# Performance work log

Hardware: AMD Instinct MI355X
Metric: run time of the kernel (lower is better)

Reference implementation:

```python
import jax, jax.numpy as jnp
import numpy as np

N_EMBD = 1024
N_HEAD = 16
HEAD_SIZE = 64


def setup_inputs() -> dict:
    key = jax.random.key(0)
    ks = jax.random.split(key, 6)
    B, T, C, H, D = 2, 2048, N_EMBD, N_HEAD, HEAD_SIZE
    s = 1.0 / np.sqrt(C)
    x = jax.random.normal(ks[0], (B, T, C), dtype=jnp.float32)
    Wq = jax.random.normal(ks[1], (H, C, D), dtype=jnp.float32) * s
    Wk = jax.random.normal(ks[2], (H, C, D), dtype=jnp.float32) * s
    Wv = jax.random.normal(ks[3], (H, C, D), dtype=jnp.float32) * s
    Wo = jax.random.normal(ks[4], (H * D, C), dtype=jnp.float32) * (1.0 / np.sqrt(H * D))
    bo = jax.random.normal(ks[5], (C,), dtype=jnp.float32) * 0.01
    return {"x": x, "Wq": Wq, "Wk": Wk, "Wv": Wv, "Wo": Wo, "bo": bo}


def reference(x, Wq, Wk, Wv, Wo, bo):
    B, T, C = x.shape
    H, _, D = Wq.shape
    # Per-head projections, batched across heads: [B,H,T,D]
    q = jnp.einsum('btc,hcd->bhtd', x, Wq)
    k = jnp.einsum('btc,hcd->bhtd', x, Wk)
    v = jnp.einsum('btc,hcd->bhtd', x, Wv)
    # NOTE: original scales by sqrt(C) = sqrt(n_embd), not sqrt(head_size)
    scale = 1.0 / jnp.sqrt(jnp.float32(C))
    att = jnp.einsum('bhtd,bhsd->bhts', q, k) * scale  # [B,H,T,T]
    causal = jnp.tril(jnp.ones((T, T), dtype=bool))
    att = jnp.where(causal, att, -jnp.inf)
    att = jax.nn.softmax(att, axis=-1)
    # dropout omitted (eval mode / deterministic reference)
    out = jnp.einsum('bhts,bhsd->bhtd', att, v)  # [B,H,T,D]
    out = out.transpose(0, 2, 1, 3).reshape(B, T, H * D)
    return out @ Wo + bo
```

## Files before the change

### kernel.cpp

```cpp
#include <hip/hip_runtime.h>
#include <hip/hip_bf16.h>


typedef __hip_bfloat16 bf16;
typedef __bf16 v8bf __attribute__((ext_vector_type(8)));
typedef float  v4f  __attribute__((ext_vector_type(4)));
typedef unsigned long long u64;
typedef unsigned int u32;

#define MFMA16(a, b, c) __builtin_amdgcn_mfma_f32_16x16x32_bf16((a), (b), (c), 0, 0, 0)

__device__ __forceinline__ bf16 f2b(float x) { return __float2bfloat16(x); }
__device__ __forceinline__ __bf16 f2braw(float x) {
  bf16 t = __float2bfloat16(x);
  return *reinterpret_cast<__bf16*>(&t);
}
__device__ __forceinline__ unsigned short f2bu(float x) {
  bf16 t = __float2bfloat16(x);
  return *reinterpret_cast<unsigned short*>(&t);
}

__device__ __forceinline__ void load16_lds(const bf16* gptr, const bf16* lptr) {
  __builtin_amdgcn_global_load_lds(
      (const __attribute__((address_space(1))) u32*)gptr,
      (__attribute__((address_space(3))) u32*)lptr, 16, 0, 0);
}

__global__ __launch_bounds__(256) void cvt_x_kernel(
    const float* __restrict__ x, bf16* __restrict__ xb)
{
  size_t i = ((size_t)blockIdx.x * 256 + threadIdx.x) * 8;
  float4 f0 = *(const float4*)(x + i);
  float4 f1 = *(const float4*)(x + i + 4);
  v8bf v;
  v[0] = f2braw(f0.x); v[1] = f2braw(f0.y); v[2] = f2braw(f0.z); v[3] = f2braw(f0.w);
  v[4] = f2braw(f1.x); v[5] = f2braw(f1.y); v[6] = f2braw(f1.z); v[7] = f2braw(f1.w);
  *(v8bf*)(xb + i) = v;
}

__global__ __launch_bounds__(256) void transpose_qkv_kernel(
    const float* __restrict__ Wq, const float* __restrict__ Wk,
    const float* __restrict__ Wv, bf16* __restrict__ wt)
{
  __shared__ float Lt[32][33];
  const int z = blockIdx.z, p = z >> 4, h = z & 15;
  const float* ib = ((p == 0) ? Wq : (p == 1) ? Wk : Wv) + (size_t)h * 65536;
  bf16* ob = wt + (size_t)z * 65536;
  const int j0 = blockIdx.x * 32;
  const int i0 = blockIdx.y * 32;
  const int tx = threadIdx.x & 31, ty = threadIdx.x >> 5;
  #pragma unroll
  for (int r = 0; r < 4; ++r)
    Lt[ty + 8 * r][tx] = ib[(size_t)(i0 + ty + 8 * r) * 64 + j0 + tx];
  __syncthreads();
  #pragma unroll
  for (int r = 0; r < 4; ++r)
    ob[(size_t)(j0 + ty + 8 * r) * 1024 + i0 + tx] = f2b(Lt[tx][ty + 8 * r]);
}

__global__ __launch_bounds__(256) void transpose_wo_kernel(
    const float* __restrict__ in, bf16* __restrict__ outp)
{
  __shared__ float Lt[32][33];
  const int j0 = blockIdx.x * 32;
  const int i0 = blockIdx.y * 32;
  const int tx = threadIdx.x & 31, ty = threadIdx.x >> 5;
  #pragma unroll
  for (int r = 0; r < 4; ++r)
    Lt[ty + 8 * r][tx] = in[(size_t)(i0 + ty + 8 * r) * 1024 + j0 + tx];
  __syncthreads();
  #pragma unroll
  for (int r = 0; r < 4; ++r)
    outp[(size_t)(j0 + ty + 8 * r) * 1024 + i0 + tx] = f2b(Lt[tx][ty + 8 * r]);
}

__global__ __launch_bounds__(256) void qkv_gemm_kernel(
    const bf16* __restrict__ xb, const bf16* __restrict__ wt,
    bf16* __restrict__ qkv)
{
  __shared__ __align__(16) bf16 Ash[128][32];
  __shared__ __align__(16) bf16 Bsh[128][32];

  const int mt = blockIdx.x, nt = blockIdx.y;
  const int tid = threadIdx.x, w = tid >> 6, lane = tid & 63;
  const int ln = lane & 15, quad = lane >> 4;
  const int wm = w >> 1, wn = w & 1;
  const int m0 = mt * 128, n0 = nt * 128;

  const v4f vzero = {0.f, 0.f, 0.f, 0.f};
  v4f acc[4][4];
  #pragma unroll
  for (int mf = 0; mf < 4; ++mf)
    #pragma unroll
    for (int nf = 0; nf < 4; ++nf) acc[mf][nf] = vzero;

  const int srow = lane >> 2, sseg = (lane & 3) * 8;
  const bf16* ga = xb + (size_t)(m0 + 32 * w + srow) * 1024 + sseg;
  const bf16* gb = wt + (size_t)(n0 + 32 * w + srow) * 1024 + sseg;

  for (int k0 = 0; k0 < 1024; k0 += 32) {
    __syncthreads();
    load16_lds(ga + k0,             &Ash[32 * w][0]);
    load16_lds(ga + 16 * 1024 + k0, &Ash[32 * w + 16][0]);
    load16_lds(gb + k0,             &Bsh[32 * w][0]);
    load16_lds(gb + 16 * 1024 + k0, &Bsh[32 * w + 16][0]);
    __syncthreads();

    v8bf af[4], bfv[4];
    #pragma unroll
    for (int mf = 0; mf < 4; ++mf)
      af[mf] = *(const v8bf*)&Ash[wm * 64 + mf * 16 + ln][quad * 8];
    #pragma unroll
    for (int nf = 0; nf < 4; ++nf)
      bfv[nf] = *(const v8bf*)&Bsh[wn * 64 + nf * 16 + ln][quad * 8];
    #pragma unroll
    for (int mf = 0; mf < 4; ++mf)
      #pragma unroll
      for (int nf = 0; nf < 4; ++nf)
        acc[mf][nf] = MFMA16(af[mf], bfv[nf], acc[mf][nf]);
  }

  const int jcol0 = n0 + wn * 64;
  const int p = jcol0 >> 10;
  const int h = (jcol0 >> 6) & 15;
  const float scale = (p == 0) ? 0.03125f : 1.0f;

  if (p < 2) {
    bf16* base = qkv + (size_t)p * 4194304 + (size_t)h * 262144;
    #pragma unroll
    for (int mf = 0; mf < 4; ++mf)
      #pragma unroll
      for (int nf = 0; nf < 4; ++nf) {
        int d = nf * 16 + ln;
        #pragma unroll
        for (int r = 0; r < 4; ++r) {
          int m = m0 + wm * 64 + mf * 16 + quad * 4 + r;
          base[(size_t)m * 64 + d] = f2b(acc[mf][nf][r] * scale);
        }
      }
  } else {
    bf16* vb = qkv + (size_t)2 * 4194304 + (size_t)h * 262144;
    #pragma unroll
    for (int mf = 0; mf < 4; ++mf) {
      int mrow = m0 + wm * 64 + mf * 16 + quad * 4;
      int bi = mrow >> 11, t0 = mrow & 2047;
      #pragma unroll
      for (int nf = 0; nf < 4; ++nf) {
        int d = nf * 16 + ln;
        u64 pk = (u64)f2bu(acc[mf][nf][0]) |
                 ((u64)f2bu(acc[mf][nf][1]) << 16) |
                 ((u64)f2bu(acc[mf][nf][2]) << 32) |
                 ((u64)f2bu(acc[mf][nf][3]) << 48);
        *(u64*)(vb + (size_t)bi * 131072 + (size_t)d * 2048 + t0) = pk;
      }
    }
  }
}

__global__ __launch_bounds__(256) void attn_kernel(
    const bf16* __restrict__ qkv, bf16* __restrict__ att)
{
  __shared__ __align__(16) bf16 Ksh0[64][32], Ksh1[64][32];
  __shared__ __align__(16) bf16 Vsh0[64][32], Vsh1[64][32];
  __shared__ __align__(16) __bf16 Psh[4][16][72];

  const int fid = blockIdx.x;
  const int lo = fid & 255, hi = fid >> 8;
  const int mt = hi ? (15 - (lo & 15)) : (lo & 15);
  const int b = hi, h = (lo >> 4) & 15;
  const int row0 = mt * 128;

  const int tid = threadIdx.x, w = tid >> 6, lane = tid & 63;
  const int ln = lane & 15, quad = lane >> 4;

  const bf16* qbase  = qkv + (size_t)h * 262144 + (size_t)b * 131072;
  const bf16* kbase  = qbase + 4194304;
  const bf16* vtbase = qbase + 8388608;

  v8bf aq[2][2];
  #pragma unroll
  for (int mc = 0; mc < 2; ++mc)
    #pragma unroll
    for (int ks = 0; ks < 2; ++ks)
      aq[mc][ks] = *(const v8bf*)(qbase +
          (size_t)(row0 + w * 32 + mc * 16 + ln) * 64 + ks * 32 + quad * 8);

  v8bf vone;
  {
    unsigned short u = 0x3F80;
    __bf16 one_e = *reinterpret_cast<__bf16*>(&u);
    #pragma unroll
    for (int j = 0; j < 8; ++j) vone[j] = one_e;
  }

  const v4f vzero = {0.f, 0.f, 0.f, 0.f};
  v4f o[2][4], lacc[2];
  #pragma unroll
  for (int mc = 0; mc < 2; ++mc) {
    lacc[mc] = vzero;
    #pragma unroll
    for (int n = 0; n < 4; ++n) o[mc][n] = vzero;
  }

  const float NEG = -30000.0f;
  const int wrow = row0 + w * 32;
  const int wk_last = (wrow + 31) >> 6;
  const int kb_end = (row0 + 127) >> 6;

  const int srow = lane >> 2, sseg = (lane & 3) * 8;

  for (int kb = 0; kb <= kb_end; ++kb) {
    __syncthreads();
    {
      const bf16* gk = kbase + (size_t)(kb * 64 + w * 16 + srow) * 64 + sseg;
      load16_lds(gk,      &Ksh0[w * 16][0]);
      load16_lds(gk + 32, &Ksh1[w * 16][0]);
      const bf16* gv = vtbase + (size_t)(w * 16 + srow) * 2048 + kb * 64 + sseg;
      load16_lds(gv,      &Vsh0[w * 16][0]);
      load16_lds(gv + 32, &Vsh1[w * 16][0]);
    }
    __syncthreads();

    if (kb <= wk_last) {
      v8bf kf[2][4], vf[2][4];
      #pragma unroll
      for (int nf = 0; nf < 4; ++nf) {
        kf[0][nf] = *(const v8bf*)&Ksh0[nf * 16 + ln][quad * 8];
        kf[1][nf] = *(const v8bf*)&Ksh1[nf * 16 + ln][quad * 8];
        vf[0][nf] = *(const v8bf*)&Vsh0[nf * 16 + ln][quad * 8];
        vf[1][nf] = *(const v8bf*)&Vsh1[nf * 16 + ln][quad * 8];
      }

      #pragma unroll
      for (int mc = 0; mc < 2; ++mc) {
        v4f s[4];
        #pragma unroll
        for (int nf = 0; nf < 4; ++nf) s[nf] = vzero;
        #pragma unroll
        for (int ks = 0; ks < 2; ++ks)
          #pragma unroll
          for (int nf = 0; nf < 4; ++nf)
            s[nf] = MFMA16(aq[mc][ks], kf[ks][nf], s[nf]);

        if (kb == wk_last) {
          int row = wrow + mc * 16 + quad * 4;
          #pragma unroll
          for (int nf = 0; nf < 4; ++nf) {
            int col = kb * 64 + nf * 16 + ln;
            #pragma unroll
            for (int r = 0; r < 4; ++r)
              if (col > row + r) s[nf][r] = NEG;
          }
        }

        #pragma unroll
        for (int nf = 0; nf < 4; ++nf)
          #pragma unroll
          for (int r = 0; r < 4; ++r)
            Psh[w][quad * 4 + r][nf * 16 + ln] = f2braw(__expf(s[nf][r]));
        __asm__ volatile("s_waitcnt lgkmcnt(0)" ::: "memory");

        #pragma unroll
        for (int ks = 0; ks < 2; ++ks) {
          v8bf pf = *(const v8bf*)&Psh[w][ln][ks * 32 + quad * 8];
          lacc[mc] = MFMA16(pf, vone, lacc[mc]);
          #pragma unroll
          for (int nf = 0; nf < 4; ++nf)
            o[mc][nf] = MFMA16(pf, vf[ks][nf], o[mc][nf]);
        }
      }
    }
  }

  #pragma unroll
  for (int mc = 0; mc < 2; ++mc) {
    v4f inv;
    #pragma unroll
    for (int r = 0; r < 4; ++r) inv[r] = 1.0f / lacc[mc][r];
    #pragma unroll
    for (int nf = 0; nf < 4; ++nf)
      #pragma unroll
      for (int r = 0; r < 4; ++r) {
        int m = b * 2048 + wrow + mc * 16 + quad * 4 + r;
        att[(size_t)m * 1024 + h * 64 + nf * 16 + ln] = f2b(o[mc][nf][r] * inv[r]);
      }
  }
}

__global__ __launch_bounds__(256) void out_gemm_kernel(
    const bf16* __restrict__ att, const bf16* __restrict__ wot,
    const float* __restrict__ bo, float* __restrict__ out)
{
  __shared__ __align__(16) bf16 Ash[128][32];
  __shared__ __align__(16) bf16 Bsh[64][32];

  const int mt = blockIdx.x, nt = blockIdx.y;
  const int tid = threadIdx.x, w = tid >> 6, lane = tid & 63;
  const int ln = lane & 15, quad = lane >> 4;
  const int wm = w >> 1, wn = w & 1;
  const int m0 = mt * 128, n0 = nt * 64;

  const v4f vzero = {0.f, 0.f, 0.f, 0.f};
  v4f acc[4][2];
  #pragma unroll
  for (int mf = 0; mf < 4; ++mf)
    #pragma unroll
    for (int nf = 0; nf < 2; ++nf) acc[mf][nf] = vzero;

  const int srow = lane >> 2, sseg = (lane & 3) * 8;
  const bf16* ga = att + (size_t)(m0 + 32 * w + srow) * 1024 + sseg;
  const bf16* gb = wot + (size_t)(n0 + 16 * w + srow) * 1024 + sseg;

  for (int k0 = 0; k0 < 1024; k0 += 32) {
    __syncthreads();
    load16_lds(ga + k0,             &Ash[32 * w][0]);
    load16_lds(ga + 16 * 1024 + k0, &Ash[32 * w + 16][0]);
    load16_lds(gb + k0,             &Bsh[16 * w][0]);
    __syncthreads();

    v8bf af[4], bfv[2];
    #pragma unroll
    for (int mf = 0; mf < 4; ++mf)
      af[mf] = *(const v8bf*)&Ash[wm * 64 + mf * 16 + ln][quad * 8];
    #pragma unroll
    for (int nf = 0; nf < 2; ++nf)
      bfv[nf] = *(const v8bf*)&Bsh[wn * 32 + nf * 16 + ln][quad * 8];
    #pragma unroll
    for (int mf = 0; mf < 4; ++mf)
      #pragma unroll
      for (int nf = 0; nf < 2; ++nf)
        acc[mf][nf] = MFMA16(af[mf], bfv[nf], acc[mf][nf]);
  }

  #pragma unroll
  for (int nf = 0; nf < 2; ++nf) {
    int j = n0 + wn * 32 + nf * 16 + ln;
    float bias = bo[j];
    #pragma unroll
    for (int mf = 0; mf < 4; ++mf)
      #pragma unroll
      for (int r = 0; r < 4; ++r) {
        int m = m0 + wm * 64 + mf * 16 + quad * 4 + r;
        out[(size_t)m * 1024 + j] = acc[mf][nf][r] + bias;
      }
  }
}

extern "C" void kernel_launch(void* const* d_in, const int* in_sizes, int n_in,
                              void* d_out, int out_size, void* d_ws, size_t ws_size,
                              hipStream_t stream) {
  const float* x  = (const float*)d_in[0];
  const float* Wq = (const float*)d_in[1];
  const float* Wk = (const float*)d_in[2];
  const float* Wv = (const float*)d_in[3];
  const float* Wo = (const float*)d_in[4];
  const float* bo = (const float*)d_in[5];
  float* out = (float*)d_out;

  bf16* xb  = (bf16*)d_ws;
  bf16* wt  = xb + 4194304;
  bf16* wot = xb + 7340032;
  bf16* qkv = xb + 8388608;
  bf16* att = xb + 20971520;

  cvt_x_kernel<<<2048, 256, 0, stream>>>(x, xb);
  transpose_qkv_kernel<<<dim3(2, 32, 48), 256, 0, stream>>>(Wq, Wk, Wv, wt);
  transpose_wo_kernel<<<dim3(32, 32), 256, 0, stream>>>(Wo, wot);

  qkv_gemm_kernel<<<dim3(32, 24), 256, 0, stream>>>(xb, wt, qkv);
  attn_kernel<<<512, 256, 0, stream>>>(qkv, att);
  out_gemm_kernel<<<dim3(32, 16), 256, 0, stream>>>(att, wot, bo, out);
}
```

Before: 192.2 us.

## Merge prep kernels, double-buffer GEMM and attention LDS, shrink attention blocks

Combines the three preprocessing kernels (x cast, QKV weight transpose, Wo transpose) into one launch. Adds double-buffered LDS staging with prefetch of the next K tile in both GEMMs and in the attention kernel, which removes one barrier per iteration. Attention now uses 128-thread blocks over 64-row query tiles with twice as many blocks, which should improve causal load balance and occupancy. LDS use per block roughly doubles, and correctness relies on the global_load_lds writes having landed by the next barrier.

```diff
diff --git a/kernel.cpp b/kernel.cpp
--- a/kernel.cpp
+++ b/kernel.cpp
@@ -26,60 +26,59 @@
       (__attribute__((address_space(3))) u32*)lptr, 16, 0, 0);
 }
 
-__global__ __launch_bounds__(256) void cvt_x_kernel(
-    const float* __restrict__ x, bf16* __restrict__ xb)
-{
-  size_t i = ((size_t)blockIdx.x * 256 + threadIdx.x) * 8;
-  float4 f0 = *(const float4*)(x + i);
-  float4 f1 = *(const float4*)(x + i + 4);
-  v8bf v;
-  v[0] = f2braw(f0.x); v[1] = f2braw(f0.y); v[2] = f2braw(f0.z); v[3] = f2braw(f0.w);
-  v[4] = f2braw(f1.x); v[5] = f2braw(f1.y); v[6] = f2braw(f1.z); v[7] = f2braw(f1.w);
-  *(v8bf*)(xb + i) = v;
-}
-
-__global__ __launch_bounds__(256) void transpose_qkv_kernel(
+__global__ __launch_bounds__(256) void prep_kernel(
+    const float* __restrict__ x,
     const float* __restrict__ Wq, const float* __restrict__ Wk,
-    const float* __restrict__ Wv, bf16* __restrict__ wt)
+    const float* __restrict__ Wv, const float* __restrict__ Wo,
+    bf16* __restrict__ xb, bf16* __restrict__ wt, bf16* __restrict__ wot)
 {
   __shared__ float Lt[32][33];
-  const int z = blockIdx.z, p = z >> 4, h = z & 15;
-  const float* ib = ((p == 0) ? Wq : (p == 1) ? Wk : Wv) + (size_t)h * 65536;
-  bf16* ob = wt + (size_t)z * 65536;
-  const int j0 = blockIdx.x * 32;
-  const int i0 = blockIdx.y * 32;
-  const int tx = threadIdx.x & 31, ty = threadIdx.x >> 5;
-  #pragma unroll
-  for (int r = 0; r < 4; ++r)
-    Lt[ty + 8 * r][tx] = ib[(size_t)(i0 + ty + 8 * r) * 64 + j0 + tx];
-  __syncthreads();
-  #pragma unroll
-  for (int r = 0; r < 4; ++r)
-    ob[(size_t)(j0 + ty + 8 * r) * 1024 + i0 + tx] = f2b(Lt[tx][ty + 8 * r]);
-}
-
-__global__ __launch_bounds__(256) void transpose_wo_kernel(
-    const float* __restrict__ in, bf16* __restrict__ outp)
-{
-  __shared__ float Lt[32][33];
-  const int j0 = blockIdx.x * 32;
-  const int i0 = blockIdx.y * 32;
-  const int tx = threadIdx.x & 31, ty = threadIdx.x >> 5;
-  #pragma unroll
-  for (int r = 0; r < 4; ++r)
-    Lt[ty + 8 * r][tx] = in[(size_t)(i0 + ty + 8 * r) * 1024 + j0 + tx];
-  __syncthreads();
-  #pragma unroll
-  for (int r = 0; r < 4; ++r)
-    outp[(size_t)(j0 + ty + 8 * r) * 1024 + i0 + tx] = f2b(Lt[tx][ty + 8 * r]);
+  const int bid = blockIdx.x, tid = threadIdx.x;
+
+  if (bid < 2048) {
+    size_t i = ((size_t)bid * 256 + tid) * 8;
+    float4 f0 = *(const float4*)(x + i);
+    float4 f1 = *(const float4*)(x + i + 4);
+    v8bf v;
+    v[0] = f2braw(f0.x); v[1] = f2braw(f0.y); v[2] = f2braw(f0.z); v[3] = f2braw(f0.w);
+    v[4] = f2braw(f1.x); v[5] = f2braw(f1.y); v[6] = f2braw(f1.z); v[7] = f2braw(f1.w);
+    *(v8bf*)(xb + i) = v;
+    return;
+  }
+  const int tx = tid & 31, ty = tid >> 5;
+  if (bid < 5120) {
+    const int idx = bid - 2048;
+    const int z = idx >> 6, rem = idx & 63;
+    const int p = z >> 4, h = z & 15;
+    const float* ib = ((p == 0) ? Wq : (p == 1) ? Wk : Wv) + (size_t)h * 65536;
+    bf16* ob = wt + (size_t)z * 65536;
+    const int j0 = (rem & 1) * 32, i0 = (rem >> 1) * 32;
+    #pragma unroll
+    for (int r = 0; r < 4; ++r)
+      Lt[ty + 8 * r][tx] = ib[(size_t)(i0 + ty + 8 * r) * 64 + j0 + tx];
+    __syncthreads();
+    #pragma unroll
+    for (int r = 0; r < 4; ++r)
+      ob[(size_t)(j0 + ty + 8 * r) * 1024 + i0 + tx] = f2b(Lt[tx][ty + 8 * r]);
+  } else {
+    const int idx = bid - 5120;
+    const int j0 = (idx & 31) * 32, i0 = (idx >> 5) * 32;
+    #pragma unroll
+    for (int r = 0; r < 4; ++r)
+      Lt[ty + 8 * r][tx] = Wo[(size_t)(i0 + ty + 8 * r) * 1024 + j0 + tx];
+    __syncthreads();
+    #pragma unroll
+    for (int r = 0; r < 4; ++r)
+      wot[(size_t)(j0 + ty + 8 * r) * 1024 + i0 + tx] = f2b(Lt[tx][ty + 8 * r]);
+  }
 }
 
 __global__ __launch_bounds__(256) void qkv_gemm_kernel(
     const bf16* __restrict__ xb, const bf16* __restrict__ wt,
     bf16* __restrict__ qkv)
 {
-  __shared__ __align__(16) bf16 Ash[128][32];
-  __shared__ __align__(16) bf16 Bsh[128][32];
+  __shared__ __align__(16) bf16 Ash[2][128][32];
+  __shared__ __align__(16) bf16 Bsh[2][128][32];
 
   const int mt = blockIdx.x, nt = blockIdx.y;
   const int tid = threadIdx.x, w = tid >> 6, lane = tid & 63;
@@ -98,21 +97,33 @@
   const bf16* ga = xb + (size_t)(m0 + 32 * w + srow) * 1024 + sseg;
   const bf16* gb = wt + (size_t)(n0 + 32 * w + srow) * 1024 + sseg;
 
-  for (int k0 = 0; k0 < 1024; k0 += 32) {
+  {
+    load16_lds(ga,             &Ash[0][32 * w][0]);
+    load16_lds(ga + 16 * 1024, &Ash[0][32 * w + 16][0]);
+    load16_lds(gb,             &Bsh[0][32 * w][0]);
+    load16_lds(gb + 16 * 1024, &Bsh[0][32 * w + 16][0]);
+  }
+
+  for (int kt = 0; kt < 32; ++kt) {
+    const int buf = kt & 1;
     __syncthreads();
-    load16_lds(ga + k0,             &Ash[32 * w][0]);
-    load16_lds(ga + 16 * 1024 + k0, &Ash[32 * w + 16][0]);
-    load16_lds(gb + k0,             &Bsh[32 * w][0]);
-    load16_lds(gb + 16 * 1024 + k0, &Bsh[32 * w + 16][0]);
-    __syncthreads();
 
     v8bf af[4], bfv[4];
     #pragma unroll
     for (int mf = 0; mf < 4; ++mf)
-      af[mf] = *(const v8bf*)&Ash[wm * 64 + mf * 16 + ln][quad * 8];
+      af[mf] = *(const v8bf*)&Ash[buf][wm * 64 + mf * 16 + ln][quad * 8];
     #pragma unroll
     for (int nf = 0; nf < 4; ++nf)
-      bfv[nf] = *(const v8bf*)&Bsh[wn * 64 + nf * 16 + ln][quad * 8];
+      bfv[nf] = *(const v8bf*)&Bsh[buf][wn * 64 + nf * 16 + ln][quad * 8];
+
+    if (kt < 31) {
+      const int k0 = (kt + 1) * 32, nb = buf ^ 1;
+      load16_lds(ga + k0,             &Ash[nb][32 * w][0]);
+      load16_lds(ga + 16 * 1024 + k0, &Ash[nb][32 * w + 16][0]);
+      load16_lds(gb + k0,             &Bsh[nb][32 * w][0]);
+      load16_lds(gb + 16 * 1024 + k0, &Bsh[nb][32 * w + 16][0]);
+    }
+
     #pragma unroll
     for (int mf = 0; mf < 4; ++mf)
       #pragma unroll
@@ -157,18 +168,19 @@
   }
 }
 
-__global__ __launch_bounds__(256) void attn_kernel(
+__global__ __launch_bounds__(128) void attn_kernel(
     const bf16* __restrict__ qkv, bf16* __restrict__ att)
 {
-  __shared__ __align__(16) bf16 Ksh0[64][32], Ksh1[64][32];
-  __shared__ __align__(16) bf16 Vsh0[64][32], Vsh1[64][32];
-  __shared__ __align__(16) __bf16 Psh[4][16][72];
+  __shared__ __align__(16) bf16 Ksh[2][2][64][32];
+  __shared__ __align__(16) bf16 Vsh[2][2][64][32];
+  __shared__ __align__(16) __bf16 Psh[2][16][72];
 
   const int fid = blockIdx.x;
-  const int lo = fid & 255, hi = fid >> 8;
-  const int mt = hi ? (15 - (lo & 15)) : (lo & 15);
-  const int b = hi, h = (lo >> 4) & 15;
-  const int row0 = mt * 128;
+  const int mtraw = fid & 31;
+  const int mt = ((fid >> 8) & 1) ? (31 - mtraw) : mtraw;
+  const int grp = (fid >> 5) & 31;
+  const int b = grp >> 4, h = grp & 15;
+  const int row0 = mt * 64;
 
   const int tid = threadIdx.x, w = tid >> 6, lane = tid & 63;
   const int ln = lane & 15, quad = lane >> 4;
@@ -177,13 +189,14 @@
   const bf16* kbase  = qbase + 4194304;
   const bf16* vtbase = qbase + 8388608;
 
+  const int wrow = row0 + w * 32;
   v8bf aq[2][2];
   #pragma unroll
   for (int mc = 0; mc < 2; ++mc)
     #pragma unroll
     for (int ks = 0; ks < 2; ++ks)
       aq[mc][ks] = *(const v8bf*)(qbase +
-          (size_t)(row0 + w * 32 + mc * 16 + ln) * 64 + ks * 32 + quad * 8);
+          (size_t)(wrow + mc * 16 + ln) * 64 + ks * 32 + quad * 8);
 
   v8bf vone;
   {
@@ -203,74 +216,83 @@
   }
 
   const float NEG = -30000.0f;
-  const int wrow = row0 + w * 32;
-  const int wk_last = (wrow + 31) >> 6;
-  const int kb_end = (row0 + 127) >> 6;
-
+  const int kb_end = mt;
   const int srow = lane >> 2, sseg = (lane & 3) * 8;
 
+  const bf16* gk0 = kbase + (size_t)(w * 32 + srow) * 64 + sseg;
+  const bf16* gv0 = vtbase + (size_t)(w * 32 + srow) * 2048 + sseg;
+
+  #define STAGE(KB, BUF)                                                     \
+    {                                                                        \
+      const bf16* gk = gk0 + (size_t)(KB) * 64 * 64;                         \
+      load16_lds(gk,            &Ksh[BUF][0][w * 32][0]);                    \
+      load16_lds(gk + 32,       &Ksh[BUF][1][w * 32][0]);                    \
+      load16_lds(gk + 1024,     &Ksh[BUF][0][w * 32 + 16][0]);               \
+      load16_lds(gk + 1056,     &Ksh[BUF][1][w * 32 + 16][0]);               \
+      const bf16* gv = gv0 + (KB) * 64;                                      \
+      load16_lds(gv,            &Vsh[BUF][0][w * 32][0]);                    \
+      load16_lds(gv + 32,       &Vsh[BUF][1][w * 32][0]);                    \
+      load16_lds(gv + 32768,    &Vsh[BUF][0][w * 32 + 16][0]);               \
+      load16_lds(gv + 32800,    &Vsh[BUF][1][w * 32 + 16][0]);               \
+    }
+
+  STAGE(0, 0)
+
   for (int kb = 0; kb <= kb_end; ++kb) {
+    const int buf = kb & 1;
     __syncthreads();
-    {
-      const bf16* gk = kbase + (size_t)(kb * 64 + w * 16 + srow) * 64 + sseg;
-      load16_lds(gk,      &Ksh0[w * 16][0]);
-      load16_lds(gk + 32, &Ksh1[w * 16][0]);
-      const bf16* gv = vtbase + (size_t)(w * 16 + srow) * 2048 + kb * 64 + sseg;
-      load16_lds(gv,      &Vsh0[w * 16][0]);
-      load16_lds(gv + 32, &Vsh1[w * 16][0]);
-    }
-    __syncthreads();
-
-    if (kb <= wk_last) {
-      v8bf kf[2][4], vf[2][4];
-      #pragma unroll
-      for (int nf = 0; nf < 4; ++nf) {
-        kf[0][nf] = *(const v8bf*)&Ksh0[nf * 16 + ln][quad * 8];
-        kf[1][nf] = *(const v8bf*)&Ksh1[nf * 16 + ln][quad * 8];
-        vf[0][nf] = *(const v8bf*)&Vsh0[nf * 16 + ln][quad * 8];
-        vf[1][nf] = *(const v8bf*)&Vsh1[nf * 16 + ln][quad * 8];
-      }
-
-      #pragma unroll
-      for (int mc = 0; mc < 2; ++mc) {
-        v4f s[4];
-        #pragma unroll
-        for (int nf = 0; nf < 4; ++nf) s[nf] = vzero;
-        #pragma unroll
-        for (int ks = 0; ks < 2; ++ks)
-          #pragma unroll
-          for (int nf = 0; nf < 4; ++nf)
-            s[nf] = MFMA16(aq[mc][ks], kf[ks][nf], s[nf]);
-
-        if (kb == wk_last) {
-          int row = wrow + mc * 16 + quad * 4;
-          #pragma unroll
-          for (int nf = 0; nf < 4; ++nf) {
-            int col = kb * 64 + nf * 16 + ln;
-            #pragma unroll
-            for (int r = 0; r < 4; ++r)
-              if (col > row + r) s[nf][r] = NEG;
-          }
-        }
-
+
+    v8bf kf[2][4], vf[2][4];
+    #pragma unroll
+    for (int nf = 0; nf < 4; ++nf) {
+      kf[0][nf] = *(const v8bf*)&Ksh[buf][0][nf * 16 + ln][quad * 8];
+      kf[1][nf] = *(const v8bf*)&Ksh[buf][1][nf * 16 + ln][quad * 8];
+      vf[0][nf] = *(const v8bf*)&Vsh[buf][0][nf * 16 + ln][quad * 8];
+      vf[1][nf] = *(const v8bf*)&Vsh[buf][1][nf * 16 + ln][quad * 8];
+    }
+
+    if (kb < kb_end) STAGE(kb + 1, buf ^ 1)
+
+    #pragma unroll
+    for (int mc = 0; mc < 2; ++mc) {
+      v4f s[4];
+      #pragma unroll
+      for (int nf = 0; nf < 4; ++nf) s[nf] = vzero;
+      #pragma unroll
+      for (int ks = 0; ks < 2; ++ks)
         #pragma unroll
         for (int nf = 0; nf < 4; ++nf)
+          s[nf] = MFMA16(aq[mc][ks], kf[ks][nf], s[nf]);
+
+      if (kb == kb_end) {
+        int row = wrow + mc * 16 + quad * 4;
+        #pragma unroll
+        for (int nf = 0; nf < 4; ++nf) {
+          int col = kb * 64 + nf * 16 + ln;
           #pragma unroll
           for (int r = 0; r < 4; ++r)
-            Psh[w][quad * 4 + r][nf * 16 + ln] = f2braw(__expf(s[nf][r]));
-        __asm__ volatile("s_waitcnt lgkmcnt(0)" ::: "memory");
-
+            if (col > row + r) s[nf][r] = NEG;
+        }
+      }
+
+      #pragma unroll
+      for (int nf = 0; nf < 4; ++nf)
         #pragma unroll
-        for (int ks = 0; ks < 2; ++ks) {
-          v8bf pf = *(const v8bf*)&Psh[w][ln][ks * 32 + quad * 8];
-          lacc[mc] = MFMA16(pf, vone, lacc[mc]);
-          #pragma unroll
-          for (int nf = 0; nf < 4; ++nf)
-            o[mc][nf] = MFMA16(pf, vf[ks][nf], o[mc][nf]);
-        }
-      }
-    }
-  }
+        for (int r = 0; r < 4; ++r)
+          Psh[w][quad * 4 + r][nf * 16 + ln] = f2braw(__expf(s[nf][r]));
+      __asm__ volatile("s_waitcnt lgkmcnt(0)" ::: "memory");
+
+      #pragma unroll
+      for (int ks = 0; ks < 2; ++ks) {
+        v8bf pf = *(const v8bf*)&Psh[w][ln][ks * 32 + quad * 8];
+        lacc[mc] = MFMA16(pf, vone, lacc[mc]);
+        #pragma unroll
+        for (int nf = 0; nf < 4; ++nf)
+          o[mc][nf] = MFMA16(pf, vf[ks][nf], o[mc][nf]);
+      }
+    }
+  }
+  #undef STAGE
 
   #pragma unroll
   for (int mc = 0; mc < 2; ++mc) {
@@ -291,8 +313,8 @@
     const bf16* __restrict__ att, const bf16* __restrict__ wot,
     const float* __restrict__ bo, float* __restrict__ out)
 {
-  __shared__ __align__(16) bf16 Ash[128][32];
-  __shared__ __align__(16) bf16 Bsh[64][32];
+  __shared__ __align__(16) bf16 Ash[2][128][32];
+  __shared__ __align__(16) bf16 Bsh[2][64][32];
 
   const int mt = blockIdx.x, nt = blockIdx.y;
   const int tid = threadIdx.x, w = tid >> 6, lane = tid & 63;
@@ -311,20 +333,31 @@
   const bf16* ga = att + (size_t)(m0 + 32 * w + srow) * 1024 + sseg;
   const bf16* gb = wot + (size_t)(n0 + 16 * w + srow) * 1024 + sseg;
 
-  for (int k0 = 0; k0 < 1024; k0 += 32) {
+  {
+    load16_lds(ga,             &Ash[0][32 * w][0]);
+    load16_lds(ga + 16 * 1024, &Ash[0][32 * w + 16][0]);
+    load16_lds(gb,             &Bsh[0][16 * w][0]);
+  }
+
+  for (int kt = 0; kt < 32; ++kt) {
+    const int buf = kt & 1;
     __syncthreads();
-    load16_lds(ga + k0,             &Ash[32 * w][0]);
-    load16_lds(ga + 16 * 1024 + k0, &Ash[32 * w + 16][0]);
-    load16_lds(gb + k0,             &Bsh[16 * w][0]);
-    __syncthreads();
 
     v8bf af[4], bfv[2];
     #pragma unroll
     for (int mf = 0; mf < 4; ++mf)
-      af[mf] = *(const v8bf*)&Ash[wm * 64 + mf * 16 + ln][quad * 8];
+      af[mf] = *(const v8bf*)&Ash[buf][wm * 64 + mf * 16 + ln][quad * 8];
     #pragma unroll
     for (int nf = 0; nf < 2; ++nf)
-      bfv[nf] = *(const v8bf*)&Bsh[wn * 32 + nf * 16 + ln][quad * 8];
+      bfv[nf] = *(const v8bf*)&Bsh[buf][wn * 32 + nf * 16 + ln][quad * 8];
+
+    if (kt < 31) {
+      const int k0 = (kt + 1) * 32, nb = buf ^ 1;
+      load16_lds(ga + k0,             &Ash[nb][32 * w][0]);
+      load16_lds(ga + 16 * 1024 + k0, &Ash[nb][32 * w + 16][0]);
+      load16_lds(gb + k0,             &Bsh[nb][16 * w][0]);
+    }
+
     #pragma unroll
     for (int mf = 0; mf < 4; ++mf)
       #pragma unroll
@@ -363,11 +396,8 @@
   bf16* qkv = xb + 8388608;
   bf16* att = xb + 20971520;
 
-  cvt_x_kernel<<<2048, 256, 0, stream>>>(x, xb);
-  transpose_qkv_kernel<<<dim3(2, 32, 48), 256, 0, stream>>>(Wq, Wk, Wv, wt);
-  transpose_wo_kernel<<<dim3(32, 32), 256, 0, stream>>>(Wo, wot);
-
+  prep_kernel<<<6144, 256, 0, stream>>>(x, Wq, Wk, Wv, Wo, xb, wt, wot);
   qkv_gemm_kernel<<<dim3(32, 24), 256, 0, stream>>>(xb, wt, qkv);
-  attn_kernel<<<512, 256, 0, stream>>>(qkv, att);
+  attn_kernel<<<1024, 128, 0, stream>>>(qkv, att);
   out_gemm_kernel<<<dim3(32, 16), 256, 0, stream>>>(att, wot, bo, out);
 }
```

Result: faster. 182.2 us (-5.2%).
